# Kernel tuning notes

Hardware: AMD Instinct MI355X
Metric: run time of the kernel (lower is better)

The kernel has to match this reference:

```python
import jax, jax.numpy as jnp
import numpy as np

N = 32768
E = 262144
OUT = 512
H = 8
DH = OUT // H


def setup_inputs() -> dict:
    key = jax.random.key(0)
    ks = jax.random.split(key, 12)
    s = 0.02
    return {
        "h": jax.random.normal(ks[0], (N, 512), dtype=jnp.float32),
        "row": jax.random.randint(ks[1], (E,), 0, N, dtype=jnp.int32),
        "col": jax.random.randint(ks[2], (E,), 0, N, dtype=jnp.int32),
        "W_in": jax.random.normal(ks[3], (512, OUT), dtype=jnp.float32) * s,
        "b_in": jnp.zeros((OUT,), dtype=jnp.float32),
        "W_q": jax.random.normal(ks[4], (OUT, OUT), dtype=jnp.float32) * s,
        "b_q": jnp.zeros((OUT,), dtype=jnp.float32),
        "W_k": jax.random.normal(ks[5], (OUT, OUT), dtype=jnp.float32) * s,
        "b_k": jnp.zeros((OUT,), dtype=jnp.float32),
        "W_v": jax.random.normal(ks[6], (OUT, OUT), dtype=jnp.float32) * s,
        "b_v": jnp.zeros((OUT,), dtype=jnp.float32),
    }


def reference(h, row, col, W_in, b_in, W_q, b_q, W_k, b_k, W_v, b_v):
    scaling = DH ** -0.5
    x = h @ W_in + b_in                                   # [N, OUT]
    q = ((x @ W_q + b_q) * scaling).reshape(N, H, DH)     # [N, H, DH]
    k = (x @ W_k + b_k).reshape(N, H, DH)
    v = (x @ W_v + b_v).reshape(N, H, DH)

    # bsddmm: per-edge, per-head attention logits only at adjacency nonzeros
    logits = jnp.einsum("ehd,ehd->eh", q[row], k[col])    # [E, H]

    # sparse row-wise softmax over each node's incident edges
    m = jax.ops.segment_max(logits, row, num_segments=N)  # [N, H]
    ex = jnp.exp(logits - m[row])                         # [E, H]
    denom = jax.ops.segment_sum(ex, row, num_segments=N)  # [N, H]
    attn = ex / denom[row]                                # [E, H]

    # bspmm: aggregate v over neighbors with sparse attention weights
    out = jax.ops.segment_sum(attn[:, :, None] * v[col], row, num_segments=N)  # [N, H, DH]
    return out
```

## Files before the change

kernel.cpp:

```cpp
#include <hip/hip_runtime.h>

#define NN 32768
#define EE 262144
#define DM 512
#define NQKV 1536
#define NHEAD 8
#define DHEAD 64

typedef unsigned short u16;
typedef unsigned int u32;
typedef __attribute__((ext_vector_type(8))) short bf16x8;
typedef __attribute__((ext_vector_type(4))) float f32x4;
typedef __attribute__((ext_vector_type(8))) u16 u16x8;
typedef __attribute__((ext_vector_type(4))) u32 u32x4;

__device__ __forceinline__ float bf2f(u16 u) {
  union { u32 i; float f; } x; x.i = ((u32)u) << 16; return x.f;
}
__device__ __forceinline__ float bflo(u32 p) {
  union { u32 i; float f; } x; x.i = p << 16; return x.f;
}
__device__ __forceinline__ float bfhi(u32 p) {
  union { u32 i; float f; } x; x.i = p & 0xFFFF0000u; return x.f;
}
__device__ __forceinline__ u16 f2bf(float f) {
  union { float f; u32 i; } x; x.f = f;
  u32 r = x.i + 0x7FFFu + ((x.i >> 16) & 1u);
  return (u16)(r >> 16);
}

__device__ __forceinline__ void load_lds16(const u16* g, u16* l) {
  __builtin_amdgcn_global_load_lds(
      (const __attribute__((address_space(1))) char*)(const void*)g,
      (__attribute__((address_space(3))) char*)(void*)l, 16, 0, 0);
}

__device__ __forceinline__ int swz(int r, int s) {
  return s ^ (r & 3) ^ ((r >> 2) & 1);
}

#define GB_CASTH 8192
#define GB_CASTW 128
#define GB_CNTD  1024
#define GB_TCW   192
#define GB_BIAS  96
__global__ void prep_all(const float* __restrict__ h, u16* __restrict__ hb,
                         const float* __restrict__ Win, u16* __restrict__ Winb,
                         const int* __restrict__ row, int* __restrict__ deg,
                         const float* __restrict__ Wq, const float* __restrict__ Wk,
                         const float* __restrict__ Wv, u16* __restrict__ At,
                         const float* __restrict__ bin, const float* __restrict__ bq,
                         const float* __restrict__ bk, const float* __restrict__ bv,
                         float* __restrict__ bias) {
  __shared__ float t[64][65];
  const int tid = threadIdx.x;
  int b = blockIdx.x;

  if (b < GB_CASTH) {
    const int i = (b * 256 + tid) * 8;
    float4 a = *(const float4*)&h[i];
    float4 c = *(const float4*)&h[i + 4];
    u16x8 o = { f2bf(a.x), f2bf(a.y), f2bf(a.z), f2bf(a.w),
                f2bf(c.x), f2bf(c.y), f2bf(c.z), f2bf(c.w) };
    *(u16x8*)&hb[i] = o;
    return;
  }
  b -= GB_CASTH;
  if (b < GB_CASTW) {
    const int i = (b * 256 + tid) * 8;
    float4 a = *(const float4*)&Win[i];
    float4 c = *(const float4*)&Win[i + 4];
    u16x8 o = { f2bf(a.x), f2bf(a.y), f2bf(a.z), f2bf(a.w),
                f2bf(c.x), f2bf(c.y), f2bf(c.z), f2bf(c.w) };
    *(u16x8*)&Winb[i] = o;
    return;
  }
  b -= GB_CASTW;
  if (b < GB_CNTD) {
    const int e = b * 256 + tid;
    atomicAdd(&deg[row[e]], 1);
    return;
  }
  b -= GB_CNTD;
  if (b < GB_TCW) {
    const int z = b / 64;
    const int r64 = b % 64;
    const float* W = (z == 0) ? Wq : (z == 1) ? Wk : Wv;
    const float scale = (z == 0) ? 0.125f : 1.0f;
    const int m0 = (r64 >> 3) * 64;
    const int j0 = (r64 & 7) * 64;
    const int tx = tid & 63, ty = tid >> 6;
#pragma unroll
    for (int i = 0; i < 16; ++i) {
      const int r = ty * 16 + i;
      t[r][tx] = W[(size_t)(m0 + r) * 512 + (j0 + tx)];
    }
    __syncthreads();
#pragma unroll
    for (int i = 0; i < 16; ++i) {
      const int j = j0 + ty * 16 + i;
      const int pr = (z == 0) ? j : (512 + 2 * j + (z - 1));
      At[(size_t)pr * 512 + (m0 + tx)] = f2bf(t[tx][ty * 16 + i] * scale);
    }
    return;
  }
  b -= GB_TCW;
  {
    const int j = (b % 6) * 256 + tid;
    const int m0 = (b / 6) * 32;
    const float* Wsel; const float* bsel; int jj; float scale = 1.0f; int pos;
    if (j < 512)       { Wsel = Wq; bsel = bq; jj = j;        scale = 0.125f; pos = j; }
    else if (j < 1024) { Wsel = Wk; bsel = bk; jj = j - 512;  pos = 512 + 2 * jj; }
    else               { Wsel = Wv; bsel = bv; jj = j - 1024; pos = 513 + 2 * jj; }
    float s0 = 0.f, s1 = 0.f, s2 = 0.f, s3 = 0.f;
#pragma unroll
    for (int m = 0; m < 32; m += 4) {
      s0 = fmaf(bin[m0 + m],     Wsel[(size_t)(m0 + m)     * 512 + jj], s0);
      s1 = fmaf(bin[m0 + m + 1], Wsel[(size_t)(m0 + m + 1) * 512 + jj], s1);
      s2 = fmaf(bin[m0 + m + 2], Wsel[(size_t)(m0 + m + 2) * 512 + jj], s2);
      s3 = fmaf(bin[m0 + m + 3], Wsel[(size_t)(m0 + m + 3) * 512 + jj], s3);
    }
    float add = ((s0 + s1) + (s2 + s3)) * scale;
    if (m0 == 0) add += bsel[jj] * scale;
    atomicAdd(&bias[pos], add);
  }
}

__global__ void scan_deg(const int* __restrict__ deg, int* __restrict__ row_ptr,
                         int* __restrict__ cursor) {
  __shared__ int sums[1024];
  const int t = threadIdx.x;
  const int base = t * 32;
  int loc[32];
  int s = 0;
#pragma unroll
  for (int i = 0; i < 32; ++i) { loc[i] = s; s += deg[base + i]; }
  sums[t] = s;
  __syncthreads();
  for (int off = 1; off < 1024; off <<= 1) {
    int v = (t >= off) ? sums[t - off] : 0;
    __syncthreads();
    sums[t] += v;
    __syncthreads();
  }
  const int excl = sums[t] - s;
#pragma unroll
  for (int i = 0; i < 32; ++i) {
    const int val = excl + loc[i];
    row_ptr[base + i] = val;
    cursor[base + i] = val;
  }
  if (t == 1023) row_ptr[NN] = sums[1023];
}

__global__ void fill_csr(const int* __restrict__ row, const int* __restrict__ col,
                         int* __restrict__ cursor, int* __restrict__ dst) {
  const int e = blockIdx.x * 256 + threadIdx.x;
  const int r = row[e];
  const int p = atomicAdd(&cursor[r], 1);
  dst[p] = col[e];
}

__global__ __launch_bounds__(256, 2) void gemm_wt(
    const u16* __restrict__ A,
    const u16* __restrict__ B,
    u16* __restrict__ C) {
  __shared__ u16 As[2][128 * 32];
  __shared__ u16 Bs[2][128 * 32];
  const int tid = threadIdx.x;
  const int lane = tid & 63;
  const int wave = tid >> 6;
  const int quad = lane >> 4;
  const int l16 = lane & 15;
  const int m0 = blockIdx.y * 128;
  const int n0 = blockIdx.x * 128;
  const int wm = (wave >> 1) * 64;
  const int wn = (wave & 1) * 64;

  const int c0 = tid, c1 = tid + 256;
  const int r0 = c0 >> 2, ko0 = swz(r0, c0 & 3) * 8;
  const int r1 = c1 >> 2, ko1 = swz(r1, c1 & 3) * 8;
  const u16* Ag0 = A + (size_t)(m0 + r0) * DM + ko0;
  const u16* Ag1 = A + (size_t)(m0 + r1) * DM + ko1;
  const u16* Bg0 = B + (size_t)(n0 + r0) * DM + ko0;
  const u16* Bg1 = B + (size_t)(n0 + r1) * DM + ko1;

  f32x4 acc[4][4];
#pragma unroll
  for (int i = 0; i < 4; ++i)
#pragma unroll
    for (int j = 0; j < 4; ++j) acc[i][j] = (f32x4){0.f, 0.f, 0.f, 0.f};

  load_lds16(Ag0, &As[0][c0 * 8]);
  load_lds16(Bg0, &Bs[0][c0 * 8]);
  load_lds16(Ag1, &As[0][c1 * 8]);
  load_lds16(Bg1, &Bs[0][c1 * 8]);
  __syncthreads();

  int cur = 0;
#pragma unroll
  for (int kt = 32; kt < DM; kt += 32) {
    load_lds16(Ag0 + kt, &As[cur ^ 1][c0 * 8]);
    load_lds16(Bg0 + kt, &Bs[cur ^ 1][c0 * 8]);
    load_lds16(Ag1 + kt, &As[cur ^ 1][c1 * 8]);
    load_lds16(Bg1 + kt, &Bs[cur ^ 1][c1 * 8]);
    bf16x8 a[4], b[4];
#pragma unroll
    for (int i = 0; i < 4; ++i) {
      const int ra = wm + i * 16 + l16;
      const int rb = wn + i * 16 + l16;
      a[i] = *(const bf16x8*)&As[cur][ra * 32 + swz(ra, quad) * 8];
      b[i] = *(const bf16x8*)&Bs[cur][rb * 32 + swz(rb, quad) * 8];
    }
#pragma unroll
    for (int mi = 0; mi < 4; ++mi)
#pragma unroll
      for (int ni = 0; ni < 4; ++ni)
        acc[mi][ni] = __builtin_amdgcn_mfma_f32_16x16x32_bf16(a[mi], b[ni], acc[mi][ni], 0, 0, 0);
    __syncthreads();
    cur ^= 1;
  }
  {
    bf16x8 a[4], b[4];
#pragma unroll
    for (int i = 0; i < 4; ++i) {
      const int ra = wm + i * 16 + l16;
      const int rb = wn + i * 16 + l16;
      a[i] = *(const bf16x8*)&As[cur][ra * 32 + swz(ra, quad) * 8];
      b[i] = *(const bf16x8*)&Bs[cur][rb * 32 + swz(rb, quad) * 8];
    }
#pragma unroll
    for (int mi = 0; mi < 4; ++mi)
#pragma unroll
      for (int ni = 0; ni < 4; ++ni)
        acc[mi][ni] = __builtin_amdgcn_mfma_f32_16x16x32_bf16(a[mi], b[ni], acc[mi][ni], 0, 0, 0);
  }

#pragma unroll
  for (int ni = 0; ni < 4; ++ni) {
    const int coln = n0 + wn + ni * 16 + l16;
#pragma unroll
    for (int mi = 0; mi < 4; ++mi) {
#pragma unroll
      for (int r = 0; r < 4; ++r) {
        const int rowm = m0 + wm + mi * 16 + quad * 4 + r;
        C[(size_t)rowm * 512 + coln] = f2bf(acc[mi][ni][r]);
      }
    }
  }
}

__global__ __launch_bounds__(256, 2) void gemm_qkv(
    const u16* __restrict__ A,
    const u16* __restrict__ B,
    const float* __restrict__ bias,
    u16* __restrict__ C) {
  __shared__ u16 As[2][128 * 32];
  __shared__ u16 Bs[2][128 * 32];
  const int tid = threadIdx.x;
  const int lane = tid & 63;
  const int wave = tid >> 6;
  const int quad = lane >> 4;
  const int l16 = lane & 15;

  const int bid = blockIdx.y * 12 + blockIdx.x;
  const int sw = (bid & 7) * 384 + (bid >> 3);
  const int bx = sw % 12;
  const int by = sw / 12;
  const int m0 = by * 128;
  const int n0 = bx * 128;
  const int wm = (wave >> 1) * 64;
  const int wn = (wave & 1) * 64;

  const int c0 = tid, c1 = tid + 256;
  const int r0 = c0 >> 2, ko0 = swz(r0, c0 & 3) * 8;
  const int r1 = c1 >> 2, ko1 = swz(r1, c1 & 3) * 8;
  const u16* Ag0 = A + (size_t)(m0 + r0) * DM + ko0;
  const u16* Ag1 = A + (size_t)(m0 + r1) * DM + ko1;
  const u16* Bg0 = B + (size_t)(n0 + r0) * DM + ko0;
  const u16* Bg1 = B + (size_t)(n0 + r1) * DM + ko1;

  f32x4 acc[4][4];
#pragma unroll
  for (int i = 0; i < 4; ++i)
#pragma unroll
    for (int j = 0; j < 4; ++j) acc[i][j] = (f32x4){0.f, 0.f, 0.f, 0.f};

  load_lds16(Ag0, &As[0][c0 * 8]);
  load_lds16(Bg0, &Bs[0][c0 * 8]);
  load_lds16(Ag1, &As[0][c1 * 8]);
  load_lds16(Bg1, &Bs[0][c1 * 8]);
  __syncthreads();

  int cur = 0;
#pragma unroll
  for (int kt = 32; kt < DM; kt += 32) {
    load_lds16(Ag0 + kt, &As[cur ^ 1][c0 * 8]);
    load_lds16(Bg0 + kt, &Bs[cur ^ 1][c0 * 8]);
    load_lds16(Ag1 + kt, &As[cur ^ 1][c1 * 8]);
    load_lds16(Bg1 + kt, &Bs[cur ^ 1][c1 * 8]);
    bf16x8 a[4], b[4];
#pragma unroll
    for (int i = 0; i < 4; ++i) {
      const int ra = wm + i * 16 + l16;
      const int rb = wn + i * 16 + l16;
      a[i] = *(const bf16x8*)&As[cur][ra * 32 + swz(ra, quad) * 8];
      b[i] = *(const bf16x8*)&Bs[cur][rb * 32 + swz(rb, quad) * 8];
    }
#pragma unroll
    for (int mi = 0; mi < 4; ++mi)
#pragma unroll
      for (int ni = 0; ni < 4; ++ni)
        acc[mi][ni] = __builtin_amdgcn_mfma_f32_16x16x32_bf16(a[mi], b[ni], acc[mi][ni], 0, 0, 0);
    __syncthreads();
    cur ^= 1;
  }
  {
    bf16x8 a[4], b[4];
#pragma unroll
    for (int i = 0; i < 4; ++i) {
      const int ra = wm + i * 16 + l16;
      const int rb = wn + i * 16 + l16;
      a[i] = *(const bf16x8*)&As[cur][ra * 32 + swz(ra, quad) * 8];
      b[i] = *(const bf16x8*)&Bs[cur][rb * 32 + swz(rb, quad) * 8];
    }
#pragma unroll
    for (int mi = 0; mi < 4; ++mi)
#pragma unroll
      for (int ni = 0; ni < 4; ++ni)
        acc[mi][ni] = __builtin_amdgcn_mfma_f32_16x16x32_bf16(a[mi], b[ni], acc[mi][ni], 0, 0, 0);
  }

#pragma unroll
  for (int ni = 0; ni < 4; ++ni) {
    const int coln = n0 + wn + ni * 16 + l16;
    const float bv = bias[coln];
#pragma unroll
    for (int mi = 0; mi < 4; ++mi) {
#pragma unroll
      for (int r = 0; r < 4; ++r) {
        const int rowm = m0 + wm + mi * 16 + quad * 4 + r;
        C[(size_t)rowm * NQKV + coln] = f2bf(acc[mi][ni][r] + bv);
      }
    }
  }
}

__global__ __launch_bounds__(256) void attn_agg(
    const u16* __restrict__ qkv16, const u32* __restrict__ qkv32,
    const int* __restrict__ row_ptr, const int* __restrict__ dst,
    float* __restrict__ out) {
  const int gt = blockIdx.x * 256 + threadIdx.x;
  const int node = gt >> 6;
  const int lane = gt & 63;
  const int beg = row_ptr[node];
  const int end = row_ptr[node + 1];

  const u16x8 qr = *(const u16x8*)&qkv16[(size_t)node * NQKV + lane * 8];
  float qf[8];
#pragma unroll
  for (int j = 0; j < 8; ++j) qf[j] = bf2f(qr[j]);

  float acc[8] = {0.f,0.f,0.f,0.f,0.f,0.f,0.f,0.f};
  float denom = 0.f;

  for (int e = beg; e < end; e += 8) {
    const int lim = end - 1;
    int idx[8];
#pragma unroll
    for (int jj = 0; jj < 8; ++jj) idx[jj] = dst[min(e + jj, lim)];
    u32 p[8][8];
#pragma unroll
    for (int jj = 0; jj < 8; ++jj) {
      const u32* pp = qkv32 + (size_t)idx[jj] * 768 + 256 + lane * 8;
      *(u32x4*)&p[jj][0] = *(const u32x4*)pp;
      *(u32x4*)&p[jj][4] = *(const u32x4*)(pp + 4);
    }
#pragma unroll
    for (int jj = 0; jj < 8; ++jj) {
      float s = 0.f;
#pragma unroll
      for (int j = 0; j < 8; ++j) s = fmaf(qf[j], bflo(p[jj][j]), s);
      s += __shfl_xor(s, 1, 64);
      s += __shfl_xor(s, 2, 64);
      s += __shfl_xor(s, 4, 64);
      const float ex = (e + jj <= lim) ? __expf(s) : 0.f;
      denom += ex;
#pragma unroll
      for (int j = 0; j < 8; ++j) acc[j] = fmaf(ex, bfhi(p[jj][j]), acc[j]);
    }
  }

  const float inv = (end > beg) ? (1.0f / denom) : 0.f;
  float4 o0 = { acc[0] * inv, acc[1] * inv, acc[2] * inv, acc[3] * inv };
  float4 o1 = { acc[4] * inv, acc[5] * inv, acc[6] * inv, acc[7] * inv };
  float* op = &out[(size_t)node * 512 + lane * 8];
  *(float4*)op = o0;
  *(float4*)(op + 4) = o1;
}

extern "C" void kernel_launch(void* const* d_in, const int* in_sizes, int n_in,
                              void* d_out, int out_size, void* d_ws, size_t ws_size,
                              hipStream_t stream) {
  const float* h   = (const float*)d_in[0];
  const int*   row = (const int*)d_in[1];
  const int*   col = (const int*)d_in[2];
  const float* Win = (const float*)d_in[3];
  const float* bin = (const float*)d_in[4];
  const float* Wq  = (const float*)d_in[5];
  const float* bq  = (const float*)d_in[6];
  const float* Wk  = (const float*)d_in[7];
  const float* bk  = (const float*)d_in[8];
  const float* Wv  = (const float*)d_in[9];
  const float* bv  = (const float*)d_in[10];
  float* out = (float*)d_out;

  char* ws = (char*)d_ws;
  u16*   qkv     = (u16*)(ws + 0);
  u16*   hb      = (u16*)(ws + 100663296);
  u16*   Wt      = (u16*)(ws + 134217728);
  float* bias    = (float*)(ws + 135790592);
  int*   deg     = (int*)(ws + 135796736);
  int*   row_ptr = (int*)(ws + 135927808);
  int*   cursor  = (int*)(ws + 136058888);
  int*   dst     = (int*)(ws + 136189960);
  u16*   At      = (u16*)(ws + 0);
  u16*   Winb    = (u16*)(ws + 1572864);

  (void)hipMemsetAsync(deg, 0, NN * sizeof(int), stream);
  (void)hipMemsetAsync(bias, 0, NQKV * sizeof(float), stream);
  hipLaunchKernelGGL(prep_all,
                     dim3(GB_CASTH + GB_CASTW + GB_CNTD + GB_TCW + GB_BIAS),
                     dim3(256), 0, stream,
                     h, hb, Win, Winb, row, deg, Wq, Wk, Wv, At,
                     bin, bq, bk, bv, bias);
  hipLaunchKernelGGL(scan_deg,  dim3(1), dim3(1024), 0, stream, deg, row_ptr, cursor);
  hipLaunchKernelGGL(fill_csr,  dim3(EE / 256), dim3(256), 0, stream, row, col, cursor, dst);
  hipLaunchKernelGGL(gemm_wt,   dim3(512 / 128, 1536 / 128), dim3(256), 0, stream, At, Winb, Wt);
  hipLaunchKernelGGL(gemm_qkv,  dim3(NQKV / 128, NN / 128), dim3(256), 0, stream, hb, Wt, bias, qkv);
  hipLaunchKernelGGL(attn_agg,  dim3((NN * 64) / 256), dim3(256), 0, stream,
                     qkv, (const u32*)qkv, row_ptr, dst, out);
}
```

Before: 339.7 us.

## Triple-buffer QKV GEMM LDS loads and shrink attention edge batch to 4

The QKV GEMM moves from a double-buffered LDS pipeline with __syncthreads to a three-stage ring. Loads are issued two k-tiles ahead, and inline s_waitcnt vmcnt plus s_barrier let one stage stay in flight while the current tile is computed. This aims to hide global-to-LDS latency behind the MFMAs, at the cost of more shared memory per block, which could lower occupancy. The attention aggregation kernel also gathers 4 neighbor rows per iteration instead of 8, which cuts register use and wasted padded loads but exposes less memory-level parallelism.

```diff
diff --git a/kernel.cpp b/kernel.cpp
--- a/kernel.cpp
+++ b/kernel.cpp
@@ -255,8 +255,8 @@
     const u16* __restrict__ B,
     const float* __restrict__ bias,
     u16* __restrict__ C) {
-  __shared__ u16 As[2][128 * 32];
-  __shared__ u16 Bs[2][128 * 32];
+  __shared__ u16 As[3][128 * 32];
+  __shared__ u16 Bs[3][128 * 32];
   const int tid = threadIdx.x;
   const int lane = tid & 63;
   const int wave = tid >> 6;
@@ -290,39 +290,31 @@
   load_lds16(Bg0, &Bs[0][c0 * 8]);
   load_lds16(Ag1, &As[0][c1 * 8]);
   load_lds16(Bg1, &Bs[0][c1 * 8]);
-  __syncthreads();
-
-  int cur = 0;
-#pragma unroll
-  for (int kt = 32; kt < DM; kt += 32) {
-    load_lds16(Ag0 + kt, &As[cur ^ 1][c0 * 8]);
-    load_lds16(Bg0 + kt, &Bs[cur ^ 1][c0 * 8]);
-    load_lds16(Ag1 + kt, &As[cur ^ 1][c1 * 8]);
-    load_lds16(Bg1 + kt, &Bs[cur ^ 1][c1 * 8]);
+  load_lds16(Ag0 + 32, &As[1][c0 * 8]);
+  load_lds16(Bg0 + 32, &Bs[1][c0 * 8]);
+  load_lds16(Ag1 + 32, &As[1][c1 * 8]);
+  load_lds16(Bg1 + 32, &Bs[1][c1 * 8]);
+
+#pragma unroll
+  for (int t = 0; t < 16; ++t) {
+    const int bt = t % 3;
+    if (t < 15) asm volatile("s_waitcnt vmcnt(4) lgkmcnt(0)\n\ts_barrier" ::: "memory");
+    else        asm volatile("s_waitcnt vmcnt(0) lgkmcnt(0)\n\ts_barrier" ::: "memory");
+    if (t < 14) {
+      const int b2 = (t + 2) % 3;
+      const int kg = (t + 2) * 32;
+      load_lds16(Ag0 + kg, &As[b2][c0 * 8]);
+      load_lds16(Bg0 + kg, &Bs[b2][c0 * 8]);
+      load_lds16(Ag1 + kg, &As[b2][c1 * 8]);
+      load_lds16(Bg1 + kg, &Bs[b2][c1 * 8]);
+    }
     bf16x8 a[4], b[4];
 #pragma unroll
     for (int i = 0; i < 4; ++i) {
       const int ra = wm + i * 16 + l16;
       const int rb = wn + i * 16 + l16;
-      a[i] = *(const bf16x8*)&As[cur][ra * 32 + swz(ra, quad) * 8];
-      b[i] = *(const bf16x8*)&Bs[cur][rb * 32 + swz(rb, quad) * 8];
-    }
-#pragma unroll
-    for (int mi = 0; mi < 4; ++mi)
-#pragma unroll
-      for (int ni = 0; ni < 4; ++ni)
-        acc[mi][ni] = __builtin_amdgcn_mfma_f32_16x16x32_bf16(a[mi], b[ni], acc[mi][ni], 0, 0, 0);
-    __syncthreads();
-    cur ^= 1;
-  }
-  {
-    bf16x8 a[4], b[4];
-#pragma unroll
-    for (int i = 0; i < 4; ++i) {
-      const int ra = wm + i * 16 + l16;
-      const int rb = wn + i * 16 + l16;
-      a[i] = *(const bf16x8*)&As[cur][ra * 32 + swz(ra, quad) * 8];
-      b[i] = *(const bf16x8*)&Bs[cur][rb * 32 + swz(rb, quad) * 8];
+      a[i] = *(const bf16x8*)&As[bt][ra * 32 + swz(ra, quad) * 8];
+      b[i] = *(const bf16x8*)&Bs[bt][rb * 32 + swz(rb, quad) * 8];
     }
 #pragma unroll
     for (int mi = 0; mi < 4; ++mi)
@@ -353,38 +345,39 @@
   const int gt = blockIdx.x * 256 + threadIdx.x;
   const int node = gt >> 6;
   const int lane = gt & 63;
+  const u16x8 qr = *(const u16x8*)&qkv16[(size_t)node * NQKV + lane * 8];
+  float qf[8];
+#pragma unroll
+  for (int j = 0; j < 8; ++j) qf[j] = bf2f(qr[j]);
+
   const int beg = row_ptr[node];
   const int end = row_ptr[node + 1];
-
-  const u16x8 qr = *(const u16x8*)&qkv16[(size_t)node * NQKV + lane * 8];
-  float qf[8];
-#pragma unroll
-  for (int j = 0; j < 8; ++j) qf[j] = bf2f(qr[j]);
-
   float acc[8] = {0.f,0.f,0.f,0.f,0.f,0.f,0.f,0.f};
   float denom = 0.f;
 
-  for (int e = beg; e < end; e += 8) {
-    const int lim = end - 1;
-    int idx[8];
-#pragma unroll
-    for (int jj = 0; jj < 8; ++jj) idx[jj] = dst[min(e + jj, lim)];
-    u32 p[8][8];
-#pragma unroll
-    for (int jj = 0; jj < 8; ++jj) {
+  for (int e = beg; e < end; e += 4) {
+    u32 p[4][8];
+    int idx[4];
+#pragma unroll
+    for (int jj = 0; jj < 4; ++jj) {
+      const int ee = min(e + jj, end - 1);
+      idx[jj] = dst[ee];
+    }
+#pragma unroll
+    for (int jj = 0; jj < 4; ++jj) {
       const u32* pp = qkv32 + (size_t)idx[jj] * 768 + 256 + lane * 8;
       *(u32x4*)&p[jj][0] = *(const u32x4*)pp;
       *(u32x4*)&p[jj][4] = *(const u32x4*)(pp + 4);
     }
 #pragma unroll
-    for (int jj = 0; jj < 8; ++jj) {
+    for (int jj = 0; jj < 4; ++jj) {
       float s = 0.f;
 #pragma unroll
       for (int j = 0; j < 8; ++j) s = fmaf(qf[j], bflo(p[jj][j]), s);
       s += __shfl_xor(s, 1, 64);
       s += __shfl_xor(s, 2, 64);
       s += __shfl_xor(s, 4, 64);
-      const float ex = (e + jj <= lim) ? __expf(s) : 0.f;
+      const float ex = (e + jj < end) ? __expf(s) : 0.f;
       denom += ex;
 #pragma unroll
       for (int j = 0; j < 8; ++j) acc[j] = fmaf(ex, bfhi(p[jj][j]), acc[j]);
```

After: 338.8 us. About the same (-0.2%).
